# Performance work log

Hardware: AMD Instinct MI355X
Metric: run time of the kernel (lower is better)

## Reference

```python
import jax, jax.numpy as jnp
import numpy as np

ATOMS_PER_RES = 24  # hard-coded in .view(B, N_l, -1, 24)
NEG_SLOPE = 0.01    # nn.LeakyReLU default


def setup_inputs() -> dict:
    key = jax.random.key(0)
    ks = jax.random.split(key, 10)
    B, N_l, N_p, H, G = 16, 64, 512, 128, 10
    pos_l = jax.random.normal(ks[0], (B, N_l, 3), jnp.float32) * 5.0
    pos_p = jax.random.normal(ks[1], (B, N_p, ATOMS_PER_RES, 3), jnp.float32) * 5.0
    Interact = jax.random.normal(ks[2], (B, N_l, N_p, H), jnp.float32)
    Interact_mask = jax.random.randint(ks[3], (B, N_l, N_p), 0, 2) > 0
    W_pi = jax.random.normal(ks[4], (H, G), jnp.float32) * 0.05
    b_pi = jnp.zeros((G,), jnp.float32)
    W_sigma = jax.random.normal(ks[5], (H, G), jnp.float32) * 0.05
    b_sigma = jnp.zeros((G,), jnp.float32)
    W_mu = jax.random.normal(ks[6], (H, G), jnp.float32) * 0.05
    b_mu = jnp.zeros((G,), jnp.float32)
    return {
        "pos_l": pos_l, "pos_p": pos_p, "Interact": Interact,
        "Interact_mask": Interact_mask,
        "W_pi": W_pi, "b_pi": b_pi,
        "W_sigma": W_sigma, "b_sigma": b_sigma,
        "W_mu": W_mu, "b_mu": b_mu,
    }


def _min_dist(pos_l, pos_p):
    # pos_l: [B, N_l, 3]; pos_p: [B, N_p, 24, 3]
    B, N_l, _ = pos_l.shape
    Y = pos_p.reshape(B, -1, 3)  # [B, N_p*24, 3]
    d2 = (jnp.sum(pos_l * pos_l, axis=-1)[..., None]
          + jnp.sum(Y * Y, axis=-1)[:, None, :]
          - 2.0 * jnp.einsum('bic,bjc->bij', pos_l, Y))  # [B, N_l, N_p*24]
    dist = jnp.nan_to_num(jnp.sqrt(d2), nan=10000.0)
    # min over the 24 atoms of each residue -> [B, N_l, N_p]
    return dist.reshape(B, N_l, -1, ATOMS_PER_RES).min(axis=-1)


def reference(pos_l, pos_p, Interact, Interact_mask,
              W_pi, b_pi, W_sigma, b_sigma, W_mu, b_mu):
    leaky = lambda x: jax.nn.leaky_relu(x, NEG_SLOPE)
    dist = _min_dist(pos_l, pos_p)                       # [B, N_l, N_p]
    # original gathers dist[Interact_mask]; keep static shape, zero-fill masked-out
    dist_masked = jnp.where(Interact_mask, dist, 0.0)
    pi = jax.nn.softmax(Interact @ W_pi + b_pi, axis=-1)          # [B,N_l,N_p,G]
    sigma = jnp.clip(leaky(Interact @ W_sigma + b_sigma) + 1.1, 1e-6, None)
    mu = leaky(Interact @ W_mu + b_mu) + 1.0
    return pi, sigma, mu, dist_masked, Interact_mask
```

## Files before the change

### kernel.cpp

```cpp
#include <hip/hip_runtime.h>
#include <cmath>

#define NB 16
#define NL 64
#define NP 512
#define NH 128
#define NG 10
#define ROWS (NB * NL * NP)

#define OFF_PI    ((size_t)0)
#define OFF_SIGMA ((size_t)5242880)
#define OFF_MU    ((size_t)10485760)
#define OFF_DIST  ((size_t)15728640)
#define OFF_MASK  ((size_t)16252928)

#define XPAD 36

__global__ __launch_bounds__(256, 4) void k_fused(
    const float* __restrict__ pos_l,
    const float* __restrict__ pos_p,
    const int*   __restrict__ mask,
    const float* __restrict__ X,
    const float* __restrict__ Wpi, const float* __restrict__ bpi,
    const float* __restrict__ Wsg, const float* __restrict__ bsg,
    const float* __restrict__ Wmu, const float* __restrict__ bmu,
    float* __restrict__ out_pi,
    float* __restrict__ out_sg,
    float* __restrict__ out_mu,
    float* __restrict__ dist_out,
    float* __restrict__ mask_out)
{
    __shared__ __align__(16) float xs[256 * XPAD];

    const int tid = threadIdx.x;
    const int idx = blockIdx.x * 256 + tid;
    const size_t row0 = (size_t)blockIdx.x * 256;

    int sr[8], sk[8];
    #pragma unroll
    for (int j = 0; j < 8; ++j) {
        int s = j * 256 + tid;
        sr[j] = s >> 3;
        sk[j] = s & 7;
    }

    float4 pf[8];
    #pragma unroll
    for (int j = 0; j < 8; ++j)
        pf[j] = *(const float4*)(X + (row0 + sr[j]) * NH + sk[j] * 4);

    {
        int p  = idx & (NP - 1);
        int bl = idx >> 9;
        int b  = bl >> 6;

        const float* xl = pos_l + bl * 3;
        float x0 = xl[0], x1 = xl[1], x2 = xl[2];
        float qs = x0 * x0 + x1 * x1 + x2 * x2;

        const float4* yp = (const float4*)(pos_p + ((size_t)(b * NP + p)) * 72);

        float m2 = 1e30f;
        #pragma unroll
        for (int q = 0; q < 6; ++q) {
            float4 v0 = yp[q * 3 + 0];
            float4 v1 = yp[q * 3 + 1];
            float4 v2 = yp[q * 3 + 2];
            float c[12] = {v0.x, v0.y, v0.z, v0.w,
                           v1.x, v1.y, v1.z, v1.w,
                           v2.x, v2.y, v2.z, v2.w};
            #pragma unroll
            for (int a = 0; a < 4; ++a) {
                float yx = c[a * 3 + 0], yy = c[a * 3 + 1], yz = c[a * 3 + 2];
                float d2 = qs + (yx * yx + yy * yy + yz * yz)
                              - 2.0f * (x0 * yx + x1 * yy + x2 * yz);
                d2 = (d2 >= 0.0f) ? d2 : 1e8f;
                m2 = fminf(m2, d2);
            }
        }
        float m = sqrtf(m2);

        int mk = mask[idx];
        dist_out[idx] = mk ? m : 0.0f;
        mask_out[idx] = mk ? 1.0f : 0.0f;
    }

    float accp[NG], accs[NG], accm[NG];
    #pragma unroll
    for (int g = 0; g < NG; ++g) {
        accp[g] = bpi[g];
        accs[g] = bsg[g];
        accm[g] = bmu[g];
    }

    for (int kc = 0; kc < 4; ++kc) {
        __syncthreads();
        #pragma unroll
        for (int j = 0; j < 8; ++j)
            *(float4*)&xs[sr[j] * XPAD + sk[j] * 4] = pf[j];
        __syncthreads();

        if (kc < 3) {
            #pragma unroll
            for (int j = 0; j < 8; ++j)
                pf[j] = *(const float4*)(X + (row0 + sr[j]) * NH
                                           + (kc + 1) * 32 + sk[j] * 4);
        }

        const float4* xr4 = (const float4*)&xs[tid * XPAD];
        #pragma unroll
        for (int k4 = 0; k4 < 8; ++k4) {
            float4 h4 = xr4[k4];
            float hk[4] = {h4.x, h4.y, h4.z, h4.w};
            #pragma unroll
            for (int kk = 0; kk < 4; ++kk) {
                int kg = kc * 32 + k4 * 4 + kk;
                const float* wp = Wpi + kg * NG;
                const float* ws = Wsg + kg * NG;
                const float* wm = Wmu + kg * NG;
                float h = hk[kk];
                #pragma unroll
                for (int g = 0; g < NG; ++g) {
                    accp[g] = fmaf(h, wp[g], accp[g]);
                    accs[g] = fmaf(h, ws[g], accs[g]);
                    accm[g] = fmaf(h, wm[g], accm[g]);
                }
            }
        }
    }

    const size_t ro = (size_t)idx * NG;

    float mx = accp[0];
    #pragma unroll
    for (int g = 1; g < NG; ++g) mx = fmaxf(mx, accp[g]);
    float e[NG], ssum = 0.0f;
    #pragma unroll
    for (int g = 0; g < NG; ++g) { e[g] = __expf(accp[g] - mx); ssum += e[g]; }
    float inv = 1.0f / ssum;
    #pragma unroll
    for (int g = 0; g < 5; ++g)
        *(float2*)&out_pi[ro + 2 * g] = make_float2(e[2 * g] * inv,
                                                    e[2 * g + 1] * inv);

    float sg[NG];
    #pragma unroll
    for (int g = 0; g < NG; ++g) {
        float x = accs[g];
        sg[g] = fmaxf((x >= 0.0f ? x : 0.01f * x) + 1.1f, 1e-6f);
    }
    #pragma unroll
    for (int g = 0; g < 5; ++g)
        *(float2*)&out_sg[ro + 2 * g] = make_float2(sg[2 * g], sg[2 * g + 1]);

    float mu[NG];
    #pragma unroll
    for (int g = 0; g < NG; ++g) {
        float x = accm[g];
        mu[g] = (x >= 0.0f ? x : 0.01f * x) + 1.0f;
    }
    #pragma unroll
    for (int g = 0; g < 5; ++g)
        *(float2*)&out_mu[ro + 2 * g] = make_float2(mu[2 * g], mu[2 * g + 1]);
}

extern "C" void kernel_launch(void* const* d_in, const int* in_sizes, int n_in,
                              void* d_out, int out_size, void* d_ws, size_t ws_size,
                              hipStream_t stream) {
    const float* pos_l    = (const float*)d_in[0];
    const float* pos_p    = (const float*)d_in[1];
    const float* Interact = (const float*)d_in[2];
    const int*   mask     = (const int*)  d_in[3];
    const float* Wpi      = (const float*)d_in[4];
    const float* bpi      = (const float*)d_in[5];
    const float* Wsg      = (const float*)d_in[6];
    const float* bsg      = (const float*)d_in[7];
    const float* Wmu      = (const float*)d_in[8];
    const float* bmu      = (const float*)d_in[9];

    float* out      = (float*)d_out;
    float* out_pi   = out + OFF_PI;
    float* out_sg   = out + OFF_SIGMA;
    float* out_mu   = out + OFF_MU;
    float* out_dist = out + OFF_DIST;
    float* out_mask = out + OFF_MASK;

    hipLaunchKernelGGL(k_fused, dim3(ROWS / 256), dim3(256), 0, stream,
                       pos_l, pos_p, mask, Interact,
                       Wpi, bpi, Wsg, bsg, Wmu, bmu,
                       out_pi, out_sg, out_mu, out_dist, out_mask);
}
```

Baseline: 467.7 us.

## Stream activation tiles straight into LDS with global_load_lds and XOR swizzle

```diff
diff --git a/kernel.cpp b/kernel.cpp
--- a/kernel.cpp
+++ b/kernel.cpp
@@ -14,8 +14,6 @@
 #define OFF_DIST  ((size_t)15728640)
 #define OFF_MASK  ((size_t)16252928)
 
-#define XPAD 36
-
 __global__ __launch_bounds__(256, 4) void k_fused(
     const float* __restrict__ pos_l,
     const float* __restrict__ pos_p,
@@ -30,25 +28,27 @@
     float* __restrict__ dist_out,
     float* __restrict__ mask_out)
 {
-    __shared__ __align__(16) float xs[256 * XPAD];
+    __shared__ __align__(16) float xs[256 * 32];
 
-    const int tid = threadIdx.x;
-    const int idx = blockIdx.x * 256 + tid;
+    const int tid  = threadIdx.x;
+    const int lane = tid & 63;
+    const int wv   = tid >> 6;
+    const int idx  = blockIdx.x * 256 + tid;
     const size_t row0 = (size_t)blockIdx.x * 256;
 
-    int sr[8], sk[8];
-    #pragma unroll
-    for (int j = 0; j < 8; ++j) {
-        int s = j * 256 + tid;
-        sr[j] = s >> 3;
-        sk[j] = s & 7;
-    }
+    const int rsub = lane >> 3;
+    const int csw  = (lane & 7) ^ rsub;
+    const float* gs = X + (row0 + 8 * wv + rsub) * NH + 4 * csw;
+    char* lb = (char*)xs + 1024 * wv;
 
-    float4 pf[8];
     #pragma unroll
     for (int j = 0; j < 8; ++j)
-        pf[j] = *(const float4*)(X + (row0 + sr[j]) * NH + sk[j] * 4);
+        __builtin_amdgcn_global_load_lds(
+            (const __attribute__((address_space(1))) void*)(gs + 4096 * j),
+            (__attribute__((address_space(3))) void*)(lb + 4096 * j),
+            16, 0, 0);
 
+    float dist_v, mask_v;
     {
         int p  = idx & (NP - 1);
         int bl = idx >> 9;
@@ -81,9 +81,11 @@
         float m = sqrtf(m2);
 
         int mk = mask[idx];
-        dist_out[idx] = mk ? m : 0.0f;
-        mask_out[idx] = mk ? 1.0f : 0.0f;
+        dist_v = mk ? m : 0.0f;
+        mask_v = mk ? 1.0f : 0.0f;
     }
+    dist_out[idx] = dist_v;
+    mask_out[idx] = mask_v;
 
     float accp[NG], accs[NG], accm[NG];
     #pragma unroll
@@ -93,31 +95,24 @@
         accm[g] = bmu[g];
     }
 
+    const float4* xr4 = (const float4*)xs + tid * 8;
+    const int sw = tid & 7;
+
     for (int kc = 0; kc < 4; ++kc) {
         __syncthreads();
+        const float* wp0 = Wpi + kc * 32 * NG;
+        const float* ws0 = Wsg + kc * 32 * NG;
+        const float* wm0 = Wmu + kc * 32 * NG;
+
         #pragma unroll
-        for (int j = 0; j < 8; ++j)
-            *(float4*)&xs[sr[j] * XPAD + sk[j] * 4] = pf[j];
-        __syncthreads();
-
-        if (kc < 3) {
-            #pragma unroll
-            for (int j = 0; j < 8; ++j)
-                pf[j] = *(const float4*)(X + (row0 + sr[j]) * NH
-                                           + (kc + 1) * 32 + sk[j] * 4);
-        }
-
-        const float4* xr4 = (const float4*)&xs[tid * XPAD];
-        #pragma unroll
-        for (int k4 = 0; k4 < 8; ++k4) {
-            float4 h4 = xr4[k4];
+        for (int j = 0; j < 8; ++j) {
+            float4 h4 = xr4[j ^ sw];
             float hk[4] = {h4.x, h4.y, h4.z, h4.w};
             #pragma unroll
             for (int kk = 0; kk < 4; ++kk) {
-                int kg = kc * 32 + k4 * 4 + kk;
-                const float* wp = Wpi + kg * NG;
-                const float* ws = Wsg + kg * NG;
-                const float* wm = Wmu + kg * NG;
+                const float* wp = wp0 + (j * 4 + kk) * NG;
+                const float* ws = ws0 + (j * 4 + kk) * NG;
+                const float* wm = wm0 + (j * 4 + kk) * NG;
                 float h = hk[kk];
                 #pragma unroll
                 for (int g = 0; g < NG; ++g) {
@@ -126,6 +121,17 @@
                     accm[g] = fmaf(h, wm[g], accm[g]);
                 }
             }
+        }
+
+        if (kc < 3) {
+            __syncthreads();
+            gs += 32;
+            #pragma unroll
+            for (int j = 0; j < 8; ++j)
+                __builtin_amdgcn_global_load_lds(
+                    (const __attribute__((address_space(1))) void*)(gs + 4096 * j),
+                    (__attribute__((address_space(3))) void*)(lb + 4096 * j),
+                    16, 0, 0);
         }
     }
 
@@ -143,25 +149,21 @@
         *(float2*)&out_pi[ro + 2 * g] = make_float2(e[2 * g] * inv,
                                                     e[2 * g + 1] * inv);
 
-    float sg[NG];
     #pragma unroll
-    for (int g = 0; g < NG; ++g) {
-        float x = accs[g];
-        sg[g] = fmaxf((x >= 0.0f ? x : 0.01f * x) + 1.1f, 1e-6f);
+    for (int g = 0; g < 5; ++g) {
+        float xa = accs[2 * g], xb = accs[2 * g + 1];
+        float va = fmaxf((xa >= 0.0f ? xa : 0.01f * xa) + 1.1f, 1e-6f);
+        float vb = fmaxf((xb >= 0.0f ? xb : 0.01f * xb) + 1.1f, 1e-6f);
+        *(float2*)&out_sg[ro + 2 * g] = make_float2(va, vb);
     }
+
     #pragma unroll
-    for (int g = 0; g < 5; ++g)
-        *(float2*)&out_sg[ro + 2 * g] = make_float2(sg[2 * g], sg[2 * g + 1]);
-
-    float mu[NG];
-    #pragma unroll
-    for (int g = 0; g < NG; ++g) {
-        float x = accm[g];
-        mu[g] = (x >= 0.0f ? x : 0.01f * x) + 1.0f;
+    for (int g = 0; g < 5; ++g) {
+        float xa = accm[2 * g], xb = accm[2 * g + 1];
+        float va = (xa >= 0.0f ? xa : 0.01f * xa) + 1.0f;
+        float vb = (xb >= 0.0f ? xb : 0.01f * xb) + 1.0f;
+        *(float2*)&out_mu[ro + 2 * g] = make_float2(va, vb);
     }
-    #pragma unroll
-    for (int g = 0; g < 5; ++g)
-        *(float2*)&out_mu[ro + 2 * g] = make_float2(mu[2 * g], mu[2 * g + 1]);
 }
 
 extern "C" void kernel_launch(void* const* d_in, const int* in_sizes, int n_in,
```

New measurement: 536.6 us. 14.7% more time.
